# Optimization experiments

Measured on AMD Instinct MI355X. Metric: run time of the kernel, lower is better.

## Reference

```python
import jax, jax.numpy as jnp
import numpy as np

B, S, D = 4, 4096, 768


def setup_inputs() -> dict:
    key = jax.random.key(0)
    kx, kk, kv, kq = jax.random.split(key, 4)
    scale = 1.0 / np.sqrt(D)
    x = jax.random.normal(kx, (B, S, D), dtype=jnp.float32)
    Wk = jax.random.normal(kk, (D, D), dtype=jnp.float32) * scale
    Wv = jax.random.normal(kv, (D, D), dtype=jnp.float32) * scale
    Wq = jax.random.normal(kq, (D, D), dtype=jnp.float32) * scale
    # nn.Parameter(torch.zeros(1)) -> use small nonzero so output depends on hrr path
    gain = jnp.full((1,), 0.1, dtype=jnp.float32)
    return {"x": x, "Wk": Wk, "Wv": Wv, "Wq": Wq, "gain": gain}


def reference(x, Wk, Wv, Wq, gain):
    # Linear projections (torch Linear: y = x @ W.T)
    k = jnp.einsum('bsd,ed->bse', x, Wk)
    v = jnp.einsum('bsd,ed->bse', x, Wv)
    q = jnp.einsum('bsd,ed->bse', x, Wq)
    d = x.shape[-1]
    # HRR binding: circular convolution in Fourier domain
    kf = jnp.fft.rfft(k, axis=-1)          # [B,S,D//2+1] complex
    vf = jnp.fft.rfft(v, axis=-1)
    qf = jnp.fft.rfft(q, axis=-1)
    # causal cumulative memory of bound key-value pairs
    mem = jnp.cumsum(kf * vf, axis=1)
    # unbind with query via circular correlation (approx inverse = conj)
    values_hat = jnp.fft.irfft(mem * jnp.conj(qf), n=d, axis=-1)
    return x + values_hat * gain
```

## Files before the change

kernel.cpp:

```cpp
#include <hip/hip_runtime.h>
#include <math.h>

#define D_DIM 768
#define NF    385
#define NSP   772
#define BATCH 4
#define SEQ   4096
#define MROWS 16384
#define KP5   800
#define SPECZ ((size_t)NSP * MROWS)

typedef __bf16 bf16x8 __attribute__((ext_vector_type(8)));
typedef float  f32x4  __attribute__((ext_vector_type(4)));

__device__ __forceinline__ void gl2lds16(const __bf16* g, __bf16* l) {
    __builtin_amdgcn_global_load_lds(
        (const __attribute__((address_space(1))) void*)g,
        (__attribute__((address_space(3))) void*)l, 16, 0, 0);
}

__global__ __launch_bounds__(256) void prologue(
    __bf16* __restrict__ FtabT, __bf16* __restrict__ GT,
    const float* __restrict__ W0, const float* __restrict__ W1,
    const float* __restrict__ W2, __bf16* __restrict__ WT,
    const float* __restrict__ x, __bf16* __restrict__ x16)
{
    const int bid = blockIdx.x;
    const int tid = threadIdx.x;
    if (bid < 1728) {
        __shared__ float tile[32][33];
        const int bz = bid / 576, rem = bid % 576;
        const int bx = rem % 24, by = rem / 24;
        const float* W = bz == 0 ? W0 : (bz == 1 ? W1 : W2);
        const int tx = tid & 31, ty = tid >> 5;
        const int e0 = bx * 32, d0 = by * 32;
        #pragma unroll
        for (int j = 0; j < 4; ++j)
            tile[ty + j*8][tx] = W[(size_t)(e0 + ty + j*8) * D_DIM + d0 + tx];
        __syncthreads();
        __bf16* WTz = WT + (size_t)bz * D_DIM * D_DIM;
        #pragma unroll
        for (int j = 0; j < 4; ++j)
            WTz[(size_t)(d0 + ty + j*8) * D_DIM + e0 + tx] = (__bf16)tile[tx][ty + j*8];
    } else if (bid < 2240) {
        int idx = (bid - 1728) * 256 + tid;
        const int stride = 512 * 256;
        const float w0 = 6.28318530717958647692f / (float)D_DIM;
        for (int i = idx; i < NF * D_DIM; i += stride) {
            int f = i / D_DIM, e = i - f * D_DIM;
            int m = (e * f) % D_DIM;
            float s, c;
            __sincosf(w0 * (float)m, &s, &c);
            FtabT[(size_t)(2*f)   * D_DIM + e] = (__bf16)c;
            FtabT[(size_t)(2*f+1) * D_DIM + e] = (__bf16)(-s);
            bool dcny = (f == 0) || (f == NF - 1);
            float w = dcny ? (1.0f / D_DIM) : (2.0f / D_DIM);
            GT[(size_t)e * KP5 + 2*f]     = (__bf16)(w * c);
            GT[(size_t)e * KP5 + 2*f + 1] = dcny ? (__bf16)0.0f : (__bf16)(-w * s);
        }
        for (int i = idx; i < 2 * D_DIM; i += stride)
            FtabT[(size_t)770 * D_DIM + i] = (__bf16)0.0f;
        for (int i = idx; i < D_DIM * (KP5 - 2 * NF); i += stride) {
            int r = i / (KP5 - 2 * NF), c = 2 * NF + (i % (KP5 - 2 * NF));
            GT[(size_t)r * KP5 + c] = (__bf16)0.0f;
        }
    } else {
        int idx = (bid - 2240) * 256 + tid;
        const int stride = 1024 * 256;
        const int total8 = MROWS * D_DIM / 8;
        const float4* x4 = (const float4*)x;
        for (int i = idx; i < total8; i += stride) {
            float4 a = x4[2*i], b = x4[2*i+1];
            bf16x8 o;
            o[0]=(__bf16)a.x; o[1]=(__bf16)a.y; o[2]=(__bf16)a.z; o[3]=(__bf16)a.w;
            o[4]=(__bf16)b.x; o[5]=(__bf16)b.y; o[6]=(__bf16)b.z; o[7]=(__bf16)b.w;
            *((bf16x8*)x16 + i) = o;
        }
    }
}

__global__ __launch_bounds__(256) void transposeO64(
    const unsigned short* __restrict__ OT, unsigned short* __restrict__ O)
{
    __shared__ unsigned short tile[64][66];
    const int tid = threadIdx.x;
    const int m0 = blockIdx.x * 64, c0 = blockIdx.y * 64;
    const int half = tid & 31, row8 = tid >> 5;
    #pragma unroll
    for (int p = 0; p < 8; ++p) {
        const int c = c0 + p * 8 + row8;
        unsigned int v = 0;
        if (c < NSP)
            v = *(const unsigned int*)(OT + (size_t)c * MROWS + m0 + half * 2);
        *(unsigned int*)&tile[p * 8 + row8][half * 2] = v;
    }
    __syncthreads();
    #pragma unroll
    for (int p = 0; p < 8; ++p) {
        const int m = m0 + p * 8 + row8;
        const int c = c0 + half * 2;
        if (c < KP5) {
            unsigned int re = tile[half * 2][p * 8 + row8];
            unsigned int im = tile[half * 2 + 1][p * 8 + row8];
            *(unsigned int*)(O + (size_t)m * KP5 + c) = (im << 16) | re;
        }
    }
}

__global__ __launch_bounds__(256) void mfma_nt(
    const __bf16* __restrict__ A, const __bf16* __restrict__ B, void* __restrict__ Cv,
    int M, int N, int K, int lda, int ldb, int ldc,
    long strideAz, long strideBz, long strideCz, int c_bf16,
    const float* __restrict__ addend, const float* __restrict__ gain)
{
    __shared__ __bf16 As[128 * 32];
    __shared__ __bf16 Bs[128 * 32];
    const int tid  = threadIdx.x;
    const int wave = tid >> 6, lane = tid & 63;
    const int lrow = lane & 15, lquad = lane >> 4;
    const int wm = wave >> 1, wn = wave & 1;
    const int m0 = blockIdx.y * 128, n0 = blockIdx.x * 128;
    const __bf16* Az = A + (size_t)blockIdx.z * strideAz;
    const __bf16* Bz = B + (size_t)blockIdx.z * strideBz;

    const int sr = tid >> 2;
    const int sc = (((tid & 3) ^ ((tid >> 3) & 3))) * 8;
    int ra0 = m0 + sr;      if (ra0 > M - 1) ra0 = M - 1;
    int ra1 = m0 + sr + 64; if (ra1 > M - 1) ra1 = M - 1;
    const int rb0 = n0 + sr, rb1 = n0 + sr + 64;
    __bf16* ldsA0 = As + wave * 512;
    __bf16* ldsA1 = As + 2048 + wave * 512;
    __bf16* ldsB0 = Bs + wave * 512;
    __bf16* ldsB1 = Bs + 2048 + wave * 512;

    const int swz = (lrow >> 1) & 3;
    const int fragcol = (lquad ^ swz) * 8;

    f32x4 acc[4][4];
    #pragma unroll
    for (int i = 0; i < 4; ++i)
        #pragma unroll
        for (int j = 0; j < 4; ++j)
            acc[i][j] = (f32x4){0.f, 0.f, 0.f, 0.f};

    for (int k0 = 0; k0 < K; k0 += 32) {
        gl2lds16(Az + (size_t)ra0 * lda + k0 + sc, ldsA0);
        gl2lds16(Az + (size_t)ra1 * lda + k0 + sc, ldsA1);
        gl2lds16(Bz + (size_t)rb0 * ldb + k0 + sc, ldsB0);
        gl2lds16(Bz + (size_t)rb1 * ldb + k0 + sc, ldsB1);
        __syncthreads();
        bf16x8 af[4], bfr[4];
        #pragma unroll
        for (int i = 0; i < 4; ++i) {
            af[i]  = *(const bf16x8*)&As[(wm*64 + i*16 + lrow) * 32 + fragcol];
            bfr[i] = *(const bf16x8*)&Bs[(wn*64 + i*16 + lrow) * 32 + fragcol];
        }
        #pragma unroll
        for (int i = 0; i < 4; ++i)
            #pragma unroll
            for (int j = 0; j < 4; ++j)
                acc[i][j] = __builtin_amdgcn_mfma_f32_16x16x32_bf16(
                    af[i], bfr[j], acc[i][j], 0, 0, 0);
        __syncthreads();
    }

    const int colb = n0 + wn * 64 + lrow;
    const int rowb = m0 + wm * 64 + lquad * 4;
    if (c_bf16) {
        __bf16* C = (__bf16*)Cv + (size_t)blockIdx.z * strideCz;
        #pragma unroll
        for (int i = 0; i < 4; ++i)
            #pragma unroll
            for (int j = 0; j < 4; ++j) {
                const int col = colb + j * 16;
                #pragma unroll
                for (int r = 0; r < 4; ++r) {
                    const int mm = rowb + i * 16 + r;
                    if (mm < M) C[(size_t)mm * ldc + col] = (__bf16)acc[i][j][r];
                }
            }
    } else if (addend) {
        float* C = (float*)Cv;
        const float g = gain[0];
        #pragma unroll
        for (int i = 0; i < 4; ++i)
            #pragma unroll
            for (int j = 0; j < 4; ++j) {
                const int col = colb + j * 16;
                #pragma unroll
                for (int r = 0; r < 4; ++r) {
                    const int mm = rowb + i * 16 + r;
                    if (mm < M) {
                        const size_t off = (size_t)mm * ldc + col;
                        C[off] = addend[off] + g * acc[i][j][r];
                    }
                }
            }
    } else {
        float* C = (float*)Cv + (size_t)blockIdx.z * strideCz;
        #pragma unroll
        for (int i = 0; i < 4; ++i)
            #pragma unroll
            for (int j = 0; j < 4; ++j) {
                const int col = colb + j * 16;
                #pragma unroll
                for (int r = 0; r < 4; ++r) {
                    const int mm = rowb + i * 16 + r;
                    if (mm < M) C[(size_t)mm * ldc + col] = acc[i][j][r];
                }
            }
    }
}

__global__ __launch_bounds__(512, 2) void mfma_nt256(
    const __bf16* __restrict__ A, const __bf16* __restrict__ B,
    __bf16* __restrict__ C, int M, int N, int K,
    int lda, int ldb, int ldc, int nyb)
{
    __shared__ __bf16 lds[65536];
    __bf16* AsBase = lds;
    __bf16* BsBase = lds + 32768;

    const int tid  = threadIdx.x;
    const int wave = tid >> 6, lane = tid & 63;
    const int lrow = lane & 15, lq = lane >> 4;
    const int wm = wave >> 2, wn = wave & 3;

    const int cpx = gridDim.x >> 3;
    const int swz = (blockIdx.x & 7) * cpx + (blockIdx.x >> 3);
    const int bx = swz / nyb, by = swz - bx * nyb;
    const int m0 = by * 256, n0 = bx * 256;
    const int NT = K >> 6;

    int srow[2], skcs[2];
    #pragma unroll
    for (int qq = 0; qq < 2; ++qq) {
        const int c = qq * 512 + tid;
        srow[qq] = c >> 3;
        skcs[qq] = ((c & 7) ^ (srow[qq] & 7)) * 8;
    }
    const int sdst0 = (wave << 6) * 8;
    const int sdst1 = (512 + (wave << 6)) * 8;

    auto stageA = [&](int t, int h) {
        __bf16* slot = AsBase + ((t & 1) * 2 + h) * 8192;
        const int k0 = t << 6;
        #pragma unroll
        for (int qq = 0; qq < 2; ++qq) {
            int gr = m0 + h * 128 + srow[qq];
            if (gr > M - 1) gr = M - 1;
            gl2lds16(A + (size_t)gr * lda + k0 + skcs[qq],
                     slot + (qq ? sdst1 : sdst0));
        }
    };
    auto stageB = [&](int t, int h) {
        __bf16* slot = BsBase + ((t & 1) * 2 + h) * 8192;
        const int k0 = t << 6;
        #pragma unroll
        for (int qq = 0; qq < 2; ++qq) {
            const int gr = n0 + h * 128 + srow[qq];
            gl2lds16(B + (size_t)gr * ldb + k0 + skcs[qq],
                     slot + (qq ? sdst1 : sdst0));
        }
    };

    int kx[2];
    #pragma unroll
    for (int s = 0; s < 2; ++s)
        kx[s] = (((s * 4 + lq) ^ (lrow & 7))) * 8;
    const int arow = lrow * 64;
    const int brow = ((wn & 1) * 64 + lrow) * 64;

    bf16x8 Af[4][2], Bf[2][2];
    f32x4 acc[8][4];
    #pragma unroll
    for (int i = 0; i < 8; ++i)
        #pragma unroll
        for (int j = 0; j < 4; ++j)
            acc[i][j] = (f32x4){0.f, 0.f, 0.f, 0.f};

    auto rdA = [&](const __bf16* slot, int mb) {
        #pragma unroll
        for (int ii = 0; ii < 4; ++ii)
            #pragma unroll
            for (int s = 0; s < 2; ++s)
                Af[ii][s] = *(const bf16x8*)(slot + arow + (mb * 4 + ii) * 1024 + kx[s]);
    };
    auto rdB = [&](const __bf16* slot, int nb) {
        #pragma unroll
        for (int jj = 0; jj < 2; ++jj)
            #pragma unroll
            for (int s = 0; s < 2; ++s)
                Bf[jj][s] = *(const bf16x8*)(slot + brow + (nb * 2 + jj) * 1024 + kx[s]);
    };
    auto mfmaQ = [&](int r0, int c0) {
        __builtin_amdgcn_s_setprio(1);
        #pragma unroll
        for (int ii = 0; ii < 4; ++ii)
            #pragma unroll
            for (int jj = 0; jj < 2; ++jj)
                #pragma unroll
                for (int s = 0; s < 2; ++s)
                    acc[r0 + ii][c0 + jj] = __builtin_amdgcn_mfma_f32_16x16x32_bf16(
                        Af[ii][s], Bf[jj][s], acc[r0 + ii][c0 + jj], 0, 0, 0);
        __builtin_amdgcn_s_setprio(0);
    };

    stageB(0, 0); stageB(0, 1); stageA(0, 0); stageA(0, 1);
    stageB(1, 0);
    asm volatile("s_waitcnt vmcnt(2)" ::: "memory");
    __builtin_amdgcn_s_barrier();
    __builtin_amdgcn_sched_barrier(0);

    for (int t = 0; t < NT; ++t) {
        const int d = t & 1;
        const __bf16* Ard = AsBase + (d * 2 + wm) * 8192;
        const __bf16* Brd = BsBase + (d * 2 + (wn >> 1)) * 8192;
        const bool p1 = (t + 1 < NT), p2 = (t + 2 < NT);

        rdA(Ard, 0); rdB(Brd, 0);
        if (p1) stageB(t + 1, 1);
        __builtin_amdgcn_s_barrier();
        mfmaQ(0, 0);
        __builtin_amdgcn_s_barrier();

        rdA(Ard, 1);
        if (p1) stageA(t + 1, 0);
        __builtin_amdgcn_s_barrier();
        mfmaQ(4, 0);
        __builtin_amdgcn_s_barrier();

        rdB(Brd, 1);
        if (p1) stageA(t + 1, 1);
        __builtin_amdgcn_s_barrier();
        mfmaQ(4, 2);
        __builtin_amdgcn_s_barrier();

        rdA(Ard, 0);
        if (p2) stageB(t + 2, 0);
        __builtin_amdgcn_s_barrier();
        mfmaQ(0, 2);
        if (p2) asm volatile("s_waitcnt vmcnt(2)" ::: "memory");
        else    asm volatile("s_waitcnt vmcnt(0)" ::: "memory");
        __builtin_amdgcn_s_barrier();
        __builtin_amdgcn_sched_barrier(0);
    }

    const int colb = n0 + wn * 64 + lrow;
    const int rowb = m0 + wm * 128 + lq * 4;
    #pragma unroll
    for (int i = 0; i < 8; ++i)
        #pragma unroll
        for (int j = 0; j < 4; ++j) {
            const int col = colb + j * 16;
            #pragma unroll
            for (int r = 0; r < 4; ++r) {
                const int mm = rowb + i * 16 + r;
                if (mm < M) C[(size_t)mm * ldc + col] = (__bf16)acc[i][j][r];
            }
        }
}

__global__ __launch_bounds__(256) void scan_blocks(__bf16* __restrict__ spec) {
    const int blk = blockIdx.x;
    const int b = blk / NF, f = blk % NF;
    const int tid = threadIdx.x;
    const int lane = tid & 63, wid = tid >> 6;
    const size_t colbase = (size_t)b * SEQ;
    __bf16* Kre = spec + (size_t)(2*f) * MROWS + colbase;
    __bf16* Kim = Kre + MROWS;
    const __bf16* Vre = Kre + SPECZ;
    const __bf16* Vim = Vre + MROWS;
    const __bf16* Qre = Kre + 2 * SPECZ;
    const __bf16* Qim = Qre + MROWS;
    const int s0 = tid * 16;

    bf16x8 kr0 = *(const bf16x8*)(Kre + s0), kr1 = *(const bf16x8*)(Kre + s0 + 8);
    bf16x8 ki0 = *(const bf16x8*)(Kim + s0), ki1 = *(const bf16x8*)(Kim + s0 + 8);
    bf16x8 vr0 = *(const bf16x8*)(Vre + s0), vr1 = *(const bf16x8*)(Vre + s0 + 8);
    bf16x8 vi0 = *(const bf16x8*)(Vim + s0), vi1 = *(const bf16x8*)(Vim + s0 + 8);

    float pr[16], pi[16];
    #pragma unroll
    for (int u = 0; u < 8; ++u) {
        float a = (float)kr0[u], bq = (float)ki0[u], c = (float)vr0[u], d = (float)vi0[u];
        pr[u] = a * c - bq * d;
        pi[u] = a * d + bq * c;
        float a1 = (float)kr1[u], b1 = (float)ki1[u], c1 = (float)vr1[u], d1 = (float)vi1[u];
        pr[8+u] = a1 * c1 - b1 * d1;
        pi[8+u] = a1 * d1 + b1 * c1;
    }
    #pragma unroll
    for (int j = 1; j < 16; ++j) { pr[j] += pr[j-1]; pi[j] += pi[j-1]; }
    const float totr = pr[15], toti = pi[15];

    float sr = totr, si = toti;
    #pragma unroll
    for (int d = 1; d < 64; d <<= 1) {
        float ur = __shfl_up(sr, d, 64);
        float ui = __shfl_up(si, d, 64);
        if (lane >= d) { sr += ur; si += ui; }
    }
    __shared__ float wsr[4], wsi[4];
    if (lane == 63) { wsr[wid] = sr; wsi[wid] = si; }
    __syncthreads();
    float baser = 0.f, basei = 0.f;
    #pragma unroll
    for (int w = 0; w < 3; ++w)
        if (w < wid) { baser += wsr[w]; basei += wsi[w]; }
    const float exr = baser + sr - totr;
    const float exi = basei + si - toti;

    bf16x8 qr0 = *(const bf16x8*)(Qre + s0), qr1 = *(const bf16x8*)(Qre + s0 + 8);
    bf16x8 qi0 = *(const bf16x8*)(Qim + s0), qi1 = *(const bf16x8*)(Qim + s0 + 8);
    bf16x8 outr0, outr1, outi0, outi1;
    #pragma unroll
    for (int u = 0; u < 8; ++u) {
        float mr = exr + pr[u],   mi = exi + pi[u];
        float qr = (float)qr0[u], qi = (float)qi0[u];
        outr0[u] = (__bf16)(mr * qr + mi * qi);
        outi0[u] = (__bf16)(mi * qr - mr * qi);
        float mr1 = exr + pr[8+u], mi1 = exi + pi[8+u];
        float qr_ = (float)qr1[u], qi_ = (float)qi1[u];
        outr1[u] = (__bf16)(mr1 * qr_ + mi1 * qi_);
        outi1[u] = (__bf16)(mi1 * qr_ - mr1 * qi_);
    }
    *(bf16x8*)(Kre + s0)     = outr0;
    *(bf16x8*)(Kre + s0 + 8) = outr1;
    *(bf16x8*)(Kim + s0)     = outi0;
    *(bf16x8*)(Kim + s0 + 8) = outi1;
}

extern "C" void kernel_launch(void* const* d_in, const int* in_sizes, int n_in,
                              void* d_out, int out_size, void* d_ws, size_t ws_size,
                              hipStream_t stream) {
    const float* x    = (const float*)d_in[0];
    const float* Wk   = (const float*)d_in[1];
    const float* Wv   = (const float*)d_in[2];
    const float* Wq   = (const float*)d_in[3];
    const float* gain = (const float*)d_in[4];
    float* out = (float*)d_out;

    __bf16* FtabT = (__bf16*)d_ws;
    __bf16* GT    = FtabT + (size_t)NSP * D_DIM;
    __bf16* WT    = GT    + (size_t)D_DIM * KP5;
    __bf16* x16   = WT    + (size_t)3 * D_DIM * D_DIM;
    __bf16* CTs   = x16   + (size_t)MROWS * D_DIM;
    __bf16* spec  = CTs   + (size_t)3 * NSP * D_DIM;
    __bf16* O     = spec  + SPECZ;

    prologue<<<3264, 256, 0, stream>>>(FtabT, GT, Wk, Wv, Wq, WT, x, x16);

    mfma_nt<<<dim3(6, 7, 3), 256, 0, stream>>>(
        FtabT, WT, CTs, NSP, D_DIM, D_DIM,
        D_DIM, D_DIM, D_DIM,
        0L, (long)D_DIM * D_DIM, (long)NSP * D_DIM, 1, nullptr, nullptr);

    mfma_nt256<<<dim3(64 * 10), 512, 0, stream>>>(
        CTs, x16, spec, 3 * NSP, MROWS, D_DIM,
        D_DIM, D_DIM, MROWS, 10);

    scan_blocks<<<BATCH * NF, 256, 0, stream>>>(spec);

    transposeO64<<<dim3(MROWS / 64, 13), 256, 0, stream>>>(
        (const unsigned short*)spec, (unsigned short*)O);

    mfma_nt<<<dim3(6, 128, 1), 256, 0, stream>>>(
        O, GT, out, MROWS, D_DIM, KP5,
        KP5, KP5, D_DIM, 0L, 0L, 0L, 0, x, gain);
}
```

Before: 293.5 us.

## Run final inverse-DFT GEMM on 256x256 kernel with fused residual epilogue

The final GEMM (O x GT -> out, with x + gain*acc) moves from the small-tile mfma_nt kernel to the 256x256 mfma_nt256 kernel. That kernel gains an fp32 epilogue that adds the residual and applies the gain. The padded K dimension grows from 800 to 832 so it is a multiple of the 64-wide K step, which also adds zero-padding work in the transpose. The quadrant order inside the main loop is also reordered so two B fragment sets are kept in registers, cutting LDS re-reads of A at the cost of extra registers.

```diff
diff --git a/kernel.cpp b/kernel.cpp
--- a/kernel.cpp
+++ b/kernel.cpp
@@ -7,7 +7,7 @@
 #define BATCH 4
 #define SEQ   4096
 #define MROWS 16384
-#define KP5   800
+#define KP5   832
 #define SPECZ ((size_t)NSP * MROWS)
 
 typedef __bf16 bf16x8 __attribute__((ext_vector_type(8)));
@@ -214,8 +214,9 @@
 
 __global__ __launch_bounds__(512, 2) void mfma_nt256(
     const __bf16* __restrict__ A, const __bf16* __restrict__ B,
-    __bf16* __restrict__ C, int M, int N, int K,
-    int lda, int ldb, int ldc, int nyb)
+    void* __restrict__ Cv, int M, int N, int K,
+    int lda, int ldb, int ldc, int nyb, int c_bf16,
+    const float* __restrict__ addend, const float* __restrict__ gain)
 {
     __shared__ __bf16 lds[65536];
     __bf16* AsBase = lds;
@@ -271,7 +272,7 @@
     const int arow = lrow * 64;
     const int brow = ((wn & 1) * 64 + lrow) * 64;
 
-    bf16x8 Af[4][2], Bf[2][2];
+    bf16x8 Af[4][2], Bf0[2][2], Bf1[2][2];
     f32x4 acc[8][4];
     #pragma unroll
     for (int i = 0; i < 8; ++i)
@@ -286,14 +287,14 @@
             for (int s = 0; s < 2; ++s)
                 Af[ii][s] = *(const bf16x8*)(slot + arow + (mb * 4 + ii) * 1024 + kx[s]);
     };
-    auto rdB = [&](const __bf16* slot, int nb) {
+    auto rdB = [&](const __bf16* slot, int nb, bf16x8 (&Bq)[2][2]) {
         #pragma unroll
         for (int jj = 0; jj < 2; ++jj)
             #pragma unroll
             for (int s = 0; s < 2; ++s)
-                Bf[jj][s] = *(const bf16x8*)(slot + brow + (nb * 2 + jj) * 1024 + kx[s]);
+                Bq[jj][s] = *(const bf16x8*)(slot + brow + (nb * 2 + jj) * 1024 + kx[s]);
     };
-    auto mfmaQ = [&](int r0, int c0) {
+    auto mfmaQ = [&](int r0, int c0, bf16x8 (&Bq)[2][2]) {
         __builtin_amdgcn_s_setprio(1);
         #pragma unroll
         for (int ii = 0; ii < 4; ++ii)
@@ -302,7 +303,7 @@
                 #pragma unroll
                 for (int s = 0; s < 2; ++s)
                     acc[r0 + ii][c0 + jj] = __builtin_amdgcn_mfma_f32_16x16x32_bf16(
-                        Af[ii][s], Bf[jj][s], acc[r0 + ii][c0 + jj], 0, 0, 0);
+                        Af[ii][s], Bq[jj][s], acc[r0 + ii][c0 + jj], 0, 0, 0);
         __builtin_amdgcn_s_setprio(0);
     };
 
@@ -318,28 +319,27 @@
         const __bf16* Brd = BsBase + (d * 2 + (wn >> 1)) * 8192;
         const bool p1 = (t + 1 < NT), p2 = (t + 2 < NT);
 
-        rdA(Ard, 0); rdB(Brd, 0);
+        rdA(Ard, 0); rdB(Brd, 0, Bf0);
         if (p1) stageB(t + 1, 1);
         __builtin_amdgcn_s_barrier();
-        mfmaQ(0, 0);
+        mfmaQ(0, 0, Bf0);
+        __builtin_amdgcn_s_barrier();
+
+        rdB(Brd, 1, Bf1);
+        if (p1) stageA(t + 1, 0);
+        __builtin_amdgcn_s_barrier();
+        mfmaQ(0, 2, Bf1);
         __builtin_amdgcn_s_barrier();
 
         rdA(Ard, 1);
-        if (p1) stageA(t + 1, 0);
-        __builtin_amdgcn_s_barrier();
-        mfmaQ(4, 0);
-        __builtin_amdgcn_s_barrier();
-
-        rdB(Brd, 1);
         if (p1) stageA(t + 1, 1);
         __builtin_amdgcn_s_barrier();
-        mfmaQ(4, 2);
-        __builtin_amdgcn_s_barrier();
-
-        rdA(Ard, 0);
+        mfmaQ(4, 2, Bf1);
+        __builtin_amdgcn_s_barrier();
+
         if (p2) stageB(t + 2, 0);
         __builtin_amdgcn_s_barrier();
-        mfmaQ(0, 2);
+        mfmaQ(4, 0, Bf0);
         if (p2) asm volatile("s_waitcnt vmcnt(2)" ::: "memory");
         else    asm volatile("s_waitcnt vmcnt(0)" ::: "memory");
         __builtin_amdgcn_s_barrier();
@@ -348,17 +348,37 @@
 
     const int colb = n0 + wn * 64 + lrow;
     const int rowb = m0 + wm * 128 + lq * 4;
-    #pragma unroll
-    for (int i = 0; i < 8; ++i)
-        #pragma unroll
-        for (int j = 0; j < 4; ++j) {
-            const int col = colb + j * 16;
-            #pragma unroll
-            for (int r = 0; r < 4; ++r) {
-                const int mm = rowb + i * 16 + r;
-                if (mm < M) C[(size_t)mm * ldc + col] = (__bf16)acc[i][j][r];
+    if (c_bf16) {
+        __bf16* C = (__bf16*)Cv;
+        #pragma unroll
+        for (int i = 0; i < 8; ++i)
+            #pragma unroll
+            for (int j = 0; j < 4; ++j) {
+                const int col = colb + j * 16;
+                #pragma unroll
+                for (int r = 0; r < 4; ++r) {
+                    const int mm = rowb + i * 16 + r;
+                    if (mm < M) C[(size_t)mm * ldc + col] = (__bf16)acc[i][j][r];
+                }
             }
-        }
+    } else {
+        float* C = (float*)Cv;
+        const float g = gain[0];
+        #pragma unroll
+        for (int i = 0; i < 8; ++i)
+            #pragma unroll
+            for (int j = 0; j < 4; ++j) {
+                const int col = colb + j * 16;
+                #pragma unroll
+                for (int r = 0; r < 4; ++r) {
+                    const int mm = rowb + i * 16 + r;
+                    if (mm < M) {
+                        const size_t off = (size_t)mm * ldc + col;
+                        C[off] = addend[off] + g * acc[i][j][r];
+                    }
+                }
+            }
+    }
 }
 
 __global__ __launch_bounds__(256) void scan_blocks(__bf16* __restrict__ spec) {
@@ -458,14 +478,14 @@
 
     mfma_nt256<<<dim3(64 * 10), 512, 0, stream>>>(
         CTs, x16, spec, 3 * NSP, MROWS, D_DIM,
-        D_DIM, D_DIM, MROWS, 10);
+        D_DIM, D_DIM, MROWS, 10, 1, nullptr, nullptr);
 
     scan_blocks<<<BATCH * NF, 256, 0, stream>>>(spec);
 
-    transposeO64<<<dim3(MROWS / 64, 13), 256, 0, stream>>>(
+    transposeO64<<<dim3(MROWS / 64, KP5 / 64), 256, 0, stream>>>(
         (const unsigned short*)spec, (unsigned short*)O);
 
-    mfma_nt<<<dim3(6, 128, 1), 256, 0, stream>>>(
+    mfma_nt256<<<dim3(3 * 64), 512, 0, stream>>>(
         O, GT, out, MROWS, D_DIM, KP5,
-        KP5, KP5, D_DIM, 0L, 0L, 0L, 0, x, gain);
-}
+        KP5, KP5, D_DIM, 64, 0, x, gain);
+}
```

After: 300.3 us. +2.3%, slower.
